# Performance work log

Hardware: AMD Instinct MI355X
Metric: run time of the kernel (lower is better)

The kernel has to match this reference:

```python
import jax, jax.numpy as jnp
import numpy as np

B, S, DIN, DQ, DK, NGL = 4, 8192, 512, 512, 512, 64


def setup_inputs() -> dict:
    key = jax.random.key(0)
    ks = jax.random.split(key, 10)
    q = jax.random.normal(ks[0], (B, S, DIN), dtype=jnp.float32)
    k = jax.random.normal(ks[1], (B, S, DIN), dtype=jnp.float32)
    v = jax.random.normal(ks[2], (B, S, DIN), dtype=jnp.float32)
    sc_in = 1.0 / np.sqrt(DIN)
    Wq = jax.random.normal(ks[3], (DQ, DIN), dtype=jnp.float32) * sc_in
    bq = jax.random.normal(ks[4], (DQ,), dtype=jnp.float32) * 0.01
    Wk = jax.random.normal(ks[5], (DK, DIN), dtype=jnp.float32) * sc_in
    bk = jax.random.normal(ks[6], (DK,), dtype=jnp.float32) * 0.01
    Wv = jax.random.normal(ks[7], (DK, DIN), dtype=jnp.float32) * sc_in
    bv = jax.random.normal(ks[8], (DK,), dtype=jnp.float32) * 0.01
    # deterministic stand-in for random.sample(range(DK), NGL): unique indices
    rng = np.random.default_rng(0)
    global_tokens = jnp.asarray(rng.choice(DK, size=NGL, replace=False), dtype=jnp.int32)
    return {"q": q, "k": k, "v": v, "Wq": Wq, "bq": bq, "Wk": Wk, "bk": bk,
            "Wv": Wv, "bv": bv, "global_tokens": global_tokens}


def _make_mask(global_tokens):
    # mask[a, b] = -inf iff a < b and neither a nor b is a global token
    idx = jnp.arange(DK)
    glb = jnp.zeros((DK,), dtype=bool).at[global_tokens].set(True)
    cond = (idx[:, None] < idx[None, :]) & (~glb[:, None]) & (~glb[None, :])
    return jnp.where(cond, -jnp.inf, 0.0).astype(jnp.float32)  # [DQ, DK]


def reference(q, k, v, Wq, bq, Wk, bk, Wv, bv, global_tokens):
    Q = q @ Wq.T + bq            # [B, S, DQ]
    K = k @ Wk.T + bk            # [B, S, DK]
    V = v @ Wv.T + bv            # [B, S, DK]
    # num = Q^T K contracting over the sequence axis -> [B, DQ, DK]
    num = jnp.einsum('bsq,bsk->bqk', Q, K)
    mask = _make_mask(global_tokens)
    denom = jnp.asarray(DK, jnp.float32) ** 0.5
    attn = jax.nn.softmax((num + mask) / denom, axis=-1)  # [B, DQ, DK]
    # attn @ V^T -> [B, DQ, S]
    out = jnp.einsum('bqk,bsk->bqs', attn, V)
    return out
```

## Files before the change

kernel.cpp:

```cpp
#include <hip/hip_runtime.h>
#include <stdint.h>

typedef short short8 __attribute__((ext_vector_type(8)));
typedef short short4v __attribute__((ext_vector_type(4)));
typedef float f32x4 __attribute__((ext_vector_type(4)));
typedef unsigned short ushort_t;

__device__ __forceinline__ unsigned short bf16_rne(float x){
  unsigned int u = __float_as_uint(x);
  return (unsigned short)((u + 0x7FFFu + ((u >> 16) & 1u)) >> 16);
}
__device__ __forceinline__ unsigned cvt_pk(float a, float b){
  unsigned r;
  asm("v_cvt_pk_bf16_f32 %0, %1, %2" : "=v"(r) : "v"(a), "v"(b));
  return r;
}
__device__ __forceinline__ void split4(float a0, float a1, float a2, float a3,
                                       unsigned &h0, unsigned &h1,
                                       unsigned &l0, unsigned &l1){
  h0 = cvt_pk(a0, a1); h1 = cvt_pk(a2, a3);
  float f0 = __uint_as_float(h0 << 16), f1 = __uint_as_float(h0 & 0xFFFF0000u);
  float f2 = __uint_as_float(h1 << 16), f3 = __uint_as_float(h1 & 0xFFFF0000u);
  l0 = cvt_pk(a0 - f0, a1 - f1); l1 = cvt_pk(a2 - f2, a3 - f3);
}
__device__ __forceinline__ uint4 hi8(float4 x, float4 y){
  uint4 h; h.x = cvt_pk(x.x, x.y); h.y = cvt_pk(x.z, x.w);
  h.z = cvt_pk(y.x, y.y); h.w = cvt_pk(y.z, y.w); return h;
}
__device__ __forceinline__ void split8(float4 x, float4 y, uint4 &h, uint4 &l){
  split4(x.x, x.y, x.z, x.w, h.x, h.y, l.x, l.y);
  split4(y.x, y.y, y.z, y.w, h.z, h.w, l.z, l.w);
}
__device__ __forceinline__ short8 comb(short4v a, short4v b){
  short8 r; r[0]=a[0]; r[1]=a[1]; r[2]=a[2]; r[3]=a[3];
  r[4]=b[0]; r[5]=b[1]; r[6]=b[2]; r[7]=b[3]; return r;
}

template<int TS, int ABF, int BBF, int NT, int EPI, int OB>
__global__ __launch_bounds__(256, 2) void gemm_bt(
    const void* __restrict__ Av, const void* __restrict__ Bv,
    void* __restrict__ Cv, const float* __restrict__ cvec,
    int tn, int K, int lda, int ldb, int ldc,
    long sA, long sB, long sC, long scv)
{
  const int bz = blockIdx.y;
  const int mt = blockIdx.x / tn, nt = blockIdx.x % tn;
  const int m0 = mt * TS, n0 = nt * TS;

  constexpr int MI   = TS / 64;
  constexpr int ROWE = TS * 32;
  constexpr int AL   = (NT == 3) ? 2 * ROWE : ROWE;
  constexpr int EL   = (TS == 128) ? 16 : 8;
  constexpr int SB   = (4 * AL > 16384) ? 4 * AL : 16384;
  __shared__ __align__(16) char SMEM[SB];
  short* Ah  = (short*)SMEM;
  short* Bh2 = (short*)(SMEM + 2 * AL);
  float* EP  = (float*)SMEM;

  const int t = threadIdx.x;
  const int lane = t & 63, wid = t >> 6;
  const int rowS = (TS == 128) ? (t >> 1) : (t >> 2);
  const int kh   = (TS == 128) ? (t & 1)  : (t & 3);
  const int wr = wid >> 1, wc = wid & 1;
  const int fr = lane & 15, fg = lane >> 4;

  f32x4 acc[2*MI][2*MI];
  const f32x4 Z = {0.f, 0.f, 0.f, 0.f};
  #pragma unroll
  for (int i = 0; i < 2*MI; i++)
    #pragma unroll
    for (int j = 0; j < 2*MI; j++) acc[i][j] = Z;

  const int wbase = rowS * 32;
  const int sw = (rowS >> 1) & 3;
  const int i0 = wbase + ((((TS == 128) ? (kh << 1) : kh) ^ sw) << 3);
  const int i1 = (TS == 128) ? (wbase + ((((kh << 1) + 1) ^ sw) << 3)) : 0;

  const float*    Afp = (const float*)Av    + sA * bz + (long)(m0 + rowS) * lda + kh * EL;
  const ushort_t* Abp = (const ushort_t*)Av + sA * bz + (long)(m0 + rowS) * lda + kh * EL;
  const float*    Bfp = (const float*)Bv    + sB * bz + (long)(n0 + rowS) * ldb + kh * EL;
  const ushort_t* Bbp = (const ushort_t*)Bv + sB * bz + (long)(n0 + rowS) * ldb + kh * EL;

  float4 a0, a1, a2, a3, b0, b1, b2, b3;
  short8 as0, as1, bs0, bs1;

  auto loadAB = [&](int kk){
    if (ABF == 0){
      const float4* pa = (const float4*)(Afp + kk);
      a0 = pa[0]; a1 = pa[1];
      if (TS == 128){ a2 = pa[2]; a3 = pa[3]; }
    } else {
      const short8* pa = (const short8*)(Abp + kk);
      as0 = pa[0]; if (TS == 128) as1 = pa[1];
    }
    if (BBF == 0){
      const float4* pb = (const float4*)(Bfp + kk);
      b0 = pb[0]; b1 = pb[1];
      if (TS == 128){ b2 = pb[2]; b3 = pb[3]; }
    } else {
      const short8* pb = (const short8*)(Bbp + kk);
      bs0 = pb[0]; if (TS == 128) bs1 = pb[1];
    }
  };

  loadAB(0);

  for (int k0 = 0; k0 < K; k0 += 32){
    __syncthreads();
    if (ABF == 0){
      if (NT == 3){
        uint4 h0, l0; split8(a0, a1, h0, l0);
        *(uint4*)&Ah[i0] = h0; *(uint4*)&Ah[i0 + ROWE] = l0;
        if (TS == 128){
          uint4 h1, l1; split8(a2, a3, h1, l1);
          *(uint4*)&Ah[i1] = h1; *(uint4*)&Ah[i1 + ROWE] = l1;
        }
      } else {
        *(uint4*)&Ah[i0] = hi8(a0, a1);
        if (TS == 128) *(uint4*)&Ah[i1] = hi8(a2, a3);
      }
    } else {
      *(short8*)&Ah[i0] = as0;
      if (TS == 128) *(short8*)&Ah[i1] = as1;
    }
    if (BBF == 0){
      if (NT == 3){
        uint4 h0, l0; split8(b0, b1, h0, l0);
        *(uint4*)&Bh2[i0] = h0; *(uint4*)&Bh2[i0 + ROWE] = l0;
        if (TS == 128){
          uint4 h1, l1; split8(b2, b3, h1, l1);
          *(uint4*)&Bh2[i1] = h1; *(uint4*)&Bh2[i1 + ROWE] = l1;
        }
      } else {
        *(uint4*)&Bh2[i0] = hi8(b0, b1);
        if (TS == 128) *(uint4*)&Bh2[i1] = hi8(b2, b3);
      }
    } else {
      *(short8*)&Bh2[i0] = bs0;
      if (TS == 128) *(short8*)&Bh2[i1] = bs1;
    }
    __syncthreads();

    loadAB((k0 + 32 < K) ? (k0 + 32) : k0);

    short8 fa[2*MI], fb[2*MI], fal[2*MI], fbl[2*MI];
    #pragma unroll
    for (int mi = 0; mi < 2*MI; mi++){
      int r = wr * (32*MI) + mi * 16 + fr;
      int idx = r * 32 + ((fg ^ ((r >> 1) & 3)) << 3);
      fa[mi] = *(const short8*)&Ah[idx];
      if (NT == 3) fal[mi] = *(const short8*)&Ah[idx + ROWE];
    }
    #pragma unroll
    for (int ni = 0; ni < 2*MI; ni++){
      int r = wc * (32*MI) + ni * 16 + fr;
      int idx = r * 32 + ((fg ^ ((r >> 1) & 3)) << 3);
      fb[ni] = *(const short8*)&Bh2[idx];
      if (NT == 3) fbl[ni] = *(const short8*)&Bh2[idx + ROWE];
    }
    #pragma unroll
    for (int mi = 0; mi < 2*MI; mi++)
      #pragma unroll
      for (int ni = 0; ni < 2*MI; ni++){
        acc[mi][ni] = __builtin_amdgcn_mfma_f32_16x16x32_bf16(fa[mi], fb[ni], acc[mi][ni], 0, 0, 0);
        if (NT == 3){
          acc[mi][ni] = __builtin_amdgcn_mfma_f32_16x16x32_bf16(fal[mi], fb[ni],  acc[mi][ni], 0, 0, 0);
          acc[mi][ni] = __builtin_amdgcn_mfma_f32_16x16x32_bf16(fa[mi],  fbl[ni], acc[mi][ni], 0, 0, 0);
        }
      }
  }

  float*    Cf = (float*)Cv    + sC * bz;
  ushort_t* Cb = (ushort_t*)Cv + sC * bz;
  if (TS == 128){
    #pragma unroll
    for (int p = 0; p < 4; p++){
      __syncthreads();
      if (wr == (p >> 1)){
        #pragma unroll
        for (int m2 = 0; m2 < 2; m2++){
          int mi = 2 * (p & 1) + m2;
          #pragma unroll
          for (int ni = 0; ni < 4; ni++)
            #pragma unroll
            for (int j = 0; j < 4; j++){
              int lr = m2 * 16 + fg * 4 + j;
              float o = acc[mi][ni][j];
              if (EPI == 1) o += cvec[scv * bz + m0 + p * 32 + lr];
              EP[lr * 128 + wc * 64 + ni * 16 + fr] = o;
            }
        }
      }
      __syncthreads();
      const int row = t >> 3, seg = t & 7;
      const float* src = EP + row * 128 + seg * 16;
      if (OB == 1){
        ushort_t* dst = Cb + (long)(m0 + p * 32 + row) * ldc + n0 + seg * 16;
        uint4 o0, o1;
        o0.x = cvt_pk(src[0], src[1]);  o0.y = cvt_pk(src[2], src[3]);
        o0.z = cvt_pk(src[4], src[5]);  o0.w = cvt_pk(src[6], src[7]);
        o1.x = cvt_pk(src[8], src[9]);  o1.y = cvt_pk(src[10], src[11]);
        o1.z = cvt_pk(src[12], src[13]); o1.w = cvt_pk(src[14], src[15]);
        *(uint4*)dst = o0; *(uint4*)(dst + 8) = o1;
      } else {
        float* dst = Cf + (long)(m0 + p * 32 + row) * ldc + n0 + seg * 16;
        #pragma unroll
        for (int c = 0; c < 4; c++)
          *(float4*)(dst + c * 4) = *(const float4*)(src + c * 4);
      }
    }
  } else {
    __syncthreads();
    #pragma unroll
    for (int mi = 0; mi < 2; mi++)
      #pragma unroll
      for (int ni = 0; ni < 2; ni++)
        #pragma unroll
        for (int j = 0; j < 4; j++){
          int lr = wr * 32 + mi * 16 + fg * 4 + j;
          float o = acc[mi][ni][j];
          if (EPI == 1) o += cvec[scv * bz + m0 + lr];
          EP[lr * 64 + wc * 32 + ni * 16 + fr] = o;
        }
    __syncthreads();
    const int row = t >> 2, seg = t & 3;
    const float* src = EP + row * 64 + seg * 16;
    if (OB == 1){
      ushort_t* dst = Cb + (long)(m0 + row) * ldc + n0 + seg * 16;
      uint4 o0, o1;
      o0.x = cvt_pk(src[0], src[1]);  o0.y = cvt_pk(src[2], src[3]);
      o0.z = cvt_pk(src[4], src[5]);  o0.w = cvt_pk(src[6], src[7]);
      o1.x = cvt_pk(src[8], src[9]);  o1.y = cvt_pk(src[10], src[11]);
      o1.z = cvt_pk(src[12], src[13]); o1.w = cvt_pk(src[14], src[15]);
      *(uint4*)dst = o0; *(uint4*)(dst + 8) = o1;
    } else {
      float* dst = Cf + (long)(m0 + row) * ldc + n0 + seg * 16;
      #pragma unroll
      for (int c = 0; c < 4; c++)
        *(float4*)(dst + c * 4) = *(const float4*)(src + c * 4);
    }
  }
}

template<int NSP>
__global__ __launch_bounds__(256, 2) void gemm1_tn(
    const float* __restrict__ q, const float* __restrict__ k,
    float* __restrict__ mtp, float* __restrict__ sqp, float* __restrict__ skp)
{
  constexpr int STEPS = 256 / NSP;
  const int b = blockIdx.z, sp = blockIdx.y;
  const int mt = blockIdx.x >> 2, nt = blockIdx.x & 3;
  const float* qb = q + (long)b * 8192 * 512;
  const float* kb = k + (long)b * 8192 * 512;

  __shared__ __align__(16) char SMEM[32768];
  unsigned char* As = (unsigned char*)SMEM;
  unsigned char* Bs = (unsigned char*)(SMEM + 16384);
  float* EP = (float*)SMEM;

  const int t = threadIdx.x;
  const int lam = t & 31, sg = t >> 5;
  const int lane = t & 63, wid = t >> 6;
  const int wr = wid >> 1, wc = wid & 1;
  const int fr = lane & 15, fg = lane >> 4;

  f32x4 acc[4][4];
  const f32x4 Z = {0.f, 0.f, 0.f, 0.f};
  #pragma unroll
  for (int i = 0; i < 4; i++)
    #pragma unroll
    for (int j = 0; j < 4; j++) acc[i][j] = Z;

  float sumk4[4] = {0.f, 0.f, 0.f, 0.f};
  float sumq4[4] = {0.f, 0.f, 0.f, 0.f};

  int wA[4];
  #pragma unroll
  for (int j = 0; j < 4; j++){
    int c = lam * 4 + j;
    int swc = ((c >> 2) ^ ((c & 3) << 1)) & 7;
    wA[j] = c * 128 + ((sg ^ swc) << 4);
  }

  const float* kbase = kb + (long)(sp * (STEPS * 32) + sg * 4) * 512 + mt * 128 + lam * 4;
  const float* qbase = qb + (long)(sp * (STEPS * 32) + sg * 4) * 512 + nt * 128 + lam * 4;

  float4 ka0 = *(const float4*)(kbase);
  float4 ka1 = *(const float4*)(kbase + 512);
  float4 ka2 = *(const float4*)(kbase + 1024);
  float4 ka3 = *(const float4*)(kbase + 1536);
  float4 qa0 = *(const float4*)(qbase);
  float4 qa1 = *(const float4*)(qbase + 512);
  float4 qa2 = *(const float4*)(qbase + 1024);
  float4 qa3 = *(const float4*)(qbase + 1536);

  for (int step = 0; step < STEPS; ++step){
    __syncthreads();
    #pragma unroll
    for (int j = 0; j < 4; j++){
      float a0 = ((const float*)&ka0)[j], a1 = ((const float*)&ka1)[j];
      float a2 = ((const float*)&ka2)[j], a3 = ((const float*)&ka3)[j];
      sumk4[j] += (a0 + a1) + (a2 + a3);
      unsigned h0, h1, l0, l1;
      split4(a0, a1, a2, a3, h0, h1, l0, l1);
      uint4 w; w.x = h0; w.y = h1; w.z = l0; w.w = l1;
      *(uint4*)(As + wA[j]) = w;
    }
    #pragma unroll
    for (int j = 0; j < 4; j++){
      float a0 = ((const float*)&qa0)[j], a1 = ((const float*)&qa1)[j];
      float a2 = ((const float*)&qa2)[j], a3 = ((const float*)&qa3)[j];
      sumq4[j] += (a0 + a1) + (a2 + a3);
      unsigned h0, h1, l0, l1;
      split4(a0, a1, a2, a3, h0, h1, l0, l1);
      uint4 w; w.x = h0; w.y = h1; w.z = l0; w.w = l1;
      *(uint4*)(Bs + wA[j]) = w;
    }
    __syncthreads();

    {
      const int nstep = (step < STEPS - 1) ? (step + 1) : step;
      const float* pK = kbase + (long)nstep * 16384;
      const float* pQ = qbase + (long)nstep * 16384;
      ka0 = *(const float4*)(pK);
      ka1 = *(const float4*)(pK + 512);
      ka2 = *(const float4*)(pK + 1024);
      ka3 = *(const float4*)(pK + 1536);
      qa0 = *(const float4*)(pQ);
      qa1 = *(const float4*)(pQ + 512);
      qa2 = *(const float4*)(pQ + 1024);
      qa3 = *(const float4*)(pQ + 1536);
    }

    short8 fa[4], fal[4], fb[4], fbl[4];
    #pragma unroll
    for (int mi = 0; mi < 4; mi++){
      int r = wr * 64 + mi * 16 + fr;
      int swc = ((r >> 2) ^ ((r & 3) << 1)) & 7;
      const unsigned char* bp = As + r * 128;
      int u0 = (((fg << 1) + 0) ^ swc) << 4;
      int u1 = (((fg << 1) + 1) ^ swc) << 4;
      fa[mi]  = comb(*(const short4v*)(bp + u0),     *(const short4v*)(bp + u1));
      fal[mi] = comb(*(const short4v*)(bp + u0 + 8), *(const short4v*)(bp + u1 + 8));
    }
    #pragma unroll
    for (int ni = 0; ni < 4; ni++){
      int r = wc * 64 + ni * 16 + fr;
      int swc = ((r >> 2) ^ ((r & 3) << 1)) & 7;
      const unsigned char* bp = Bs + r * 128;
      int u0 = (((fg << 1) + 0) ^ swc) << 4;
      int u1 = (((fg << 1) + 1) ^ swc) << 4;
      fb[ni]  = comb(*(const short4v*)(bp + u0),     *(const short4v*)(bp + u1));
      fbl[ni] = comb(*(const short4v*)(bp + u0 + 8), *(const short4v*)(bp + u1 + 8));
    }
    #pragma unroll
    for (int mi = 0; mi < 4; mi++)
      #pragma unroll
      for (int ni = 0; ni < 4; ni++){
        acc[mi][ni] = __builtin_amdgcn_mfma_f32_16x16x32_bf16(fa[mi],  fb[ni],  acc[mi][ni], 0, 0, 0);
        acc[mi][ni] = __builtin_amdgcn_mfma_f32_16x16x32_bf16(fal[mi], fb[ni],  acc[mi][ni], 0, 0, 0);
        acc[mi][ni] = __builtin_amdgcn_mfma_f32_16x16x32_bf16(fa[mi],  fbl[ni], acc[mi][ni], 0, 0, 0);
      }
  }

  float* Cp = mtp + ((long)sp * 4 + b) * (512 * 512);
  #pragma unroll
  for (int p = 0; p < 4; p++){
    __syncthreads();
    if (wr == (p >> 1)){
      #pragma unroll
      for (int m2 = 0; m2 < 2; m2++){
        int mi = 2 * (p & 1) + m2;
        #pragma unroll
        for (int ni = 0; ni < 4; ni++)
          #pragma unroll
          for (int j = 0; j < 4; j++){
            int lr = m2 * 16 + fg * 4 + j;
            EP[lr * 128 + wc * 64 + ni * 16 + fr] = acc[mi][ni][j];
          }
      }
    }
    __syncthreads();
    const int row = t >> 3, seg = t & 7;
    const float* src = EP + row * 128 + seg * 16;
    float* dst = Cp + (long)(mt * 128 + p * 32 + row) * 512 + nt * 128 + seg * 16;
    #pragma unroll
    for (int c = 0; c < 4; c++)
      *(float4*)(dst + c * 4) = *(const float4*)(src + c * 4);
  }

  __syncthreads();
  float* red = (float*)SMEM;
  if (mt == 0){
    #pragma unroll
    for (int j = 0; j < 4; j++) red[sg * 128 + lam * 4 + j] = sumq4[j];
    __syncthreads();
    if (t < 128){
      float s2 = 0.f;
      #pragma unroll
      for (int gg = 0; gg < 8; gg++) s2 += red[gg * 128 + t];
      sqp[((long)b * NSP + sp) * 512 + nt * 128 + t] = s2;
    }
    __syncthreads();
  }
  if (nt == 0){
    #pragma unroll
    for (int j = 0; j < 4; j++) red[sg * 128 + lam * 4 + j] = sumk4[j];
    __syncthreads();
    if (t < 128){
      float s2 = 0.f;
      #pragma unroll
      for (int gg = 0; gg < 8; gg++) s2 += red[gg * 128 + t];
      skp[((long)b * NSP + sp) * 512 + mt * 128 + t] = s2;
    }
  }
}

template<int NS>
__global__ __launch_bounds__(256) void reduceM(float* __restrict__ p){
  const int bid = blockIdx.x;
  const int b = bid >> 8;
  const long i = (long)(bid & 255) * 1024 + threadIdx.x * 4;
  float4 s = {0.f, 0.f, 0.f, 0.f};
  #pragma unroll
  for (int j = 0; j < NS; j++){
    float4 v = *(const float4*)(p + ((long)j * 4 + b) * 262144 + i);
    s.x += v.x; s.y += v.y; s.z += v.z; s.w += v.w;
  }
  *(float4*)(p + (long)b * 262144 + i) = s;
}

__global__ __launch_bounds__(256) void transpose512(const float* __restrict__ in, float* __restrict__ outp){
  __shared__ float tile[32][33];
  const int bx = blockIdx.x & 15, by = blockIdx.x >> 4;
  const int tx = threadIdx.x & 31, ty = threadIdx.x >> 5;
  #pragma unroll
  for (int r = 0; r < 4; r++)
    tile[ty + 8*r][tx] = in[(long)(by*32 + ty + 8*r) * 512 + bx*32 + tx];
  __syncthreads();
  #pragma unroll
  for (int r = 0; r < 4; r++)
    outp[(long)(bx*32 + ty + 8*r) * 512 + by*32 + tx] = tile[tx][ty + 8*r];
}

__global__ __launch_bounds__(256) void smallprep(
    const float* __restrict__ sqp, const float* __restrict__ skp,
    const float* __restrict__ Wq, const float* __restrict__ Wk,
    float* __restrict__ wqsq, float* __restrict__ wksk, int nsp)
{
  const int bid = blockIdx.x;
  const int tau = bid >> 4;
  const int b = (bid >> 2) & 3, ab = bid & 3;
  const float* P = tau ? skp : sqp;
  const float* W = tau ? Wk : Wq;
  float* O = tau ? wksk : wqsq;
  __shared__ float sv[512];
  const int t = threadIdx.x;
  for (int i = t; i < 512; i += 256){
    float s = 0.f;
    for (int g = 0; g < nsp; g++) s += P[((long)b * nsp + g) * 512 + i];
    sv[i] = s;
  }
  __syncthreads();
  const int a = ab * 128 + (t >> 1), half = t & 1;
  const float* Wr = W + (long)a * 512 + half * 256;
  const float* sp2 = sv + half * 256;
  float d = 0.f;
  #pragma unroll 8
  for (int j = 0; j < 256; j++) d += Wr[j] * sp2[j];
  d += __shfl_xor(d, 1);
  if (!half) O[(long)b * 512 + a] = d;
}

__global__ __launch_bounds__(256) void softmax_k(
    const float* __restrict__ num, float* __restrict__ attn, float* __restrict__ cv,
    const float* __restrict__ wqsq, const float* __restrict__ wksk,
    const float* __restrict__ bq, const float* __restrict__ bk,
    const float* __restrict__ bv, const int* __restrict__ gt)
{
  const int a = blockIdx.x, b = blockIdx.y;
  const int t = threadIdx.x;
  const int lane = t & 63, wid = t >> 6;
  __shared__ unsigned char gf[512];
  __shared__ float red[4];
  gf[t] = 0; gf[t + 256] = 0;
  __syncthreads();
  if (t < 64) gf[gt[t]] = 1;
  __syncthreads();

  const float* row = num + ((long)b * 512 + a) * 512;
  const float bqa = bq[a], wqa = wqsq[b * 512 + a];
  const int ga = gf[a];
  const int c0 = t, c1 = t + 256;
  float l0 = (row[c0] + wqa * bk[c0] + bqa * wksk[b*512 + c0] + 8192.0f * bqa * bk[c0]) * 0.04419417382415922f;
  float l1 = (row[c1] + wqa * bk[c1] + bqa * wksk[b*512 + c1] + 8192.0f * bqa * bk[c1]) * 0.04419417382415922f;
  if (a < c0 && !ga && !gf[c0]) l0 = -1e30f;
  if (a < c1 && !ga && !gf[c1]) l1 = -1e30f;

  float m = fmaxf(l0, l1);
  #pragma unroll
  for (int o = 32; o; o >>= 1) m = fmaxf(m, __shfl_xor(m, o));
  if (lane == 0) red[wid] = m;
  __syncthreads();
  m = fmaxf(fmaxf(red[0], red[1]), fmaxf(red[2], red[3]));
  __syncthreads();

  float e0 = __expf(l0 - m), e1 = __expf(l1 - m);
  float s = e0 + e1;
  #pragma unroll
  for (int o = 32; o; o >>= 1) s += __shfl_xor(s, o);
  if (lane == 0) red[wid] = s;
  __syncthreads();
  s = red[0] + red[1] + red[2] + red[3];
  __syncthreads();
  const float inv = 1.0f / s;
  const float a0 = e0 * inv, a1 = e1 * inv;
  float* arow = attn + ((long)b * 512 + a) * 512;
  arow[c0] = a0; arow[c1] = a1;

  float cp = a0 * bv[c0] + a1 * bv[c1];
  #pragma unroll
  for (int o = 32; o; o >>= 1) cp += __shfl_xor(cp, o);
  if (lane == 0) red[wid] = cp;
  __syncthreads();
  if (t == 0) cv[(long)b * 512 + a] = red[0] + red[1] + red[2] + red[3];
}

extern "C" void kernel_launch(void* const* d_in, const int* in_sizes, int n_in,
                              void* d_out, int out_size, void* d_ws, size_t ws_size,
                              hipStream_t stream) {
  const float* q  = (const float*)d_in[0];
  const float* k  = (const float*)d_in[1];
  const float* v  = (const float*)d_in[2];
  const float* Wq = (const float*)d_in[3];
  const float* bq = (const float*)d_in[4];
  const float* Wk = (const float*)d_in[5];
  const float* bk = (const float*)d_in[6];
  const float* Wv = (const float*)d_in[7];
  const float* bv = (const float*)d_in[8];
  const int*   gt = (const int*)d_in[9];
  float* out = (float*)d_out;

  const int NSP = 8;

  float* w = (float*)d_ws;
  float* MT   = w;
  float* T1   = w + 1048576;
  float* NUM  = w + 2097152;
  float* ATT  = w + 3145728;
  float* A2H  = w + 4194304;
  float* WVT  = A2H + 524288;
  float* SM   = w + (long)NSP * 1048576;
  float* SQP  = SM;
  float* SKP  = SQP + 32768;
  float* WQS  = SKP + 32768;
  float* WKS  = WQS + 2048;
  float* CV   = WKS + 2048;
  ushort_t* a2h = (ushort_t*)A2H;

  gemm1_tn<8><<<dim3(16, 8, 4), 256, 0, stream>>>(q, k, w, SQP, SKP);
  reduceM<8><<<1024, 256, 0, stream>>>(w);
  transpose512<<<256, 256, 0, stream>>>(Wv, WVT);
  smallprep<<<32, 256, 0, stream>>>(SQP, SKP, Wq, Wk, WQS, WKS, NSP);
  gemm_bt<64,0,0,3,0,0><<<dim3(64, 4), 256, 0, stream>>>(Wq, MT, T1, nullptr,
      8, 512, 512, 512, 512, 0L, 262144L, 262144L, 0L);
  gemm_bt<64,0,0,3,0,0><<<dim3(64, 4), 256, 0, stream>>>(T1, Wk, NUM, nullptr,
      8, 512, 512, 512, 512, 262144L, 0L, 262144L, 0L);
  softmax_k<<<dim3(512, 4), 256, 0, stream>>>(NUM, ATT, CV, WQS, WKS, bq, bk, bv, gt);
  gemm_bt<64,0,0,1,0,1><<<dim3(64, 4), 256, 0, stream>>>(ATT, WVT, a2h, nullptr,
      8, 512, 512, 512, 512, 262144L, 0L, 262144L, 0L);
  gemm_bt<128,1,0,1,1,0><<<dim3(256, 4), 256, 0, stream>>>(a2h, v, out, CV,
      64, 512, 512, 512, 8192, 262144L, 4194304L, 4194304L, 512L);
}
```

Measured before the change: 210.2 us.

## Process two K-chunks per barrier pair with doubled register prefetch in GEMMs

Both the generic gemm_bt and the gemm1_tn kernels now keep two sets of prefetched global tiles in registers and stage two 32-wide K slices into shared memory per iteration. This halves the number of __syncthreads pairs and gives more MFMA work between barriers. gemm1_tn also drops the LDS-staged epilogue and writes accumulators directly to global memory with scattered scalar stores. In exchange, register pressure and shared-memory use double (64KB in gemm1_tn), which may reduce occupancy below the launch bound of 2 blocks, and the direct stores are less coalesced.

Result: faster. 198.7 us (-5.5%).

```diff
diff --git a/kernel.cpp b/kernel.cpp
--- a/kernel.cpp
+++ b/kernel.cpp
@@ -49,12 +49,13 @@
 
   constexpr int MI   = TS / 64;
   constexpr int ROWE = TS * 32;
-  constexpr int AL   = (NT == 3) ? 2 * ROWE : ROWE;
+  constexpr int PL   = (NT == 3) ? 2 * ROWE : ROWE;
+  constexpr int TBYT = 4 * PL;
+  constexpr int SB   = (2 * TBYT > 16384) ? 2 * TBYT : 16384;
   constexpr int EL   = (TS == 128) ? 16 : 8;
-  constexpr int SB   = (4 * AL > 16384) ? 4 * AL : 16384;
   __shared__ __align__(16) char SMEM[SB];
   short* Ah  = (short*)SMEM;
-  short* Bh2 = (short*)(SMEM + 2 * AL);
+  short* Bh2 = (short*)(SMEM + TBYT);
   float* EP  = (float*)SMEM;
 
   const int t = threadIdx.x;
@@ -81,93 +82,106 @@
   const float*    Bfp = (const float*)Bv    + sB * bz + (long)(n0 + rowS) * ldb + kh * EL;
   const ushort_t* Bbp = (const ushort_t*)Bv + sB * bz + (long)(n0 + rowS) * ldb + kh * EL;
 
-  float4 a0, a1, a2, a3, b0, b1, b2, b3;
-  short8 as0, as1, bs0, bs1;
-
-  auto loadAB = [&](int kk){
+  struct Pf { float4 v[4]; };
+  struct Ps { short8 v[2]; };
+  Pf Af[2], Bf[2]; Ps As8[2], Bs8[2];
+
+  auto loadA = [&](int s, int kk){
     if (ABF == 0){
-      const float4* pa = (const float4*)(Afp + kk);
-      a0 = pa[0]; a1 = pa[1];
-      if (TS == 128){ a2 = pa[2]; a3 = pa[3]; }
+      const float4* p = (const float4*)(Afp + kk);
+      Af[s].v[0] = p[0]; Af[s].v[1] = p[1];
+      if (TS == 128){ Af[s].v[2] = p[2]; Af[s].v[3] = p[3]; }
     } else {
-      const short8* pa = (const short8*)(Abp + kk);
-      as0 = pa[0]; if (TS == 128) as1 = pa[1];
-    }
+      const short8* p = (const short8*)(Abp + kk);
+      As8[s].v[0] = p[0]; if (TS == 128) As8[s].v[1] = p[1];
+    }
+  };
+  auto loadB = [&](int s, int kk){
     if (BBF == 0){
-      const float4* pb = (const float4*)(Bfp + kk);
-      b0 = pb[0]; b1 = pb[1];
-      if (TS == 128){ b2 = pb[2]; b3 = pb[3]; }
+      const float4* p = (const float4*)(Bfp + kk);
+      Bf[s].v[0] = p[0]; Bf[s].v[1] = p[1];
+      if (TS == 128){ Bf[s].v[2] = p[2]; Bf[s].v[3] = p[3]; }
     } else {
-      const short8* pb = (const short8*)(Bbp + kk);
-      bs0 = pb[0]; if (TS == 128) bs1 = pb[1];
-    }
-  };
-
-  loadAB(0);
-
-  for (int k0 = 0; k0 < K; k0 += 32){
-    __syncthreads();
+      const short8* p = (const short8*)(Bbp + kk);
+      Bs8[s].v[0] = p[0]; if (TS == 128) Bs8[s].v[1] = p[1];
+    }
+  };
+
+  auto stage = [&](int s){
+    const int off = s * PL;
     if (ABF == 0){
       if (NT == 3){
-        uint4 h0, l0; split8(a0, a1, h0, l0);
-        *(uint4*)&Ah[i0] = h0; *(uint4*)&Ah[i0 + ROWE] = l0;
+        uint4 h0, l0; split8(Af[s].v[0], Af[s].v[1], h0, l0);
+        *(uint4*)&Ah[off + i0] = h0; *(uint4*)&Ah[off + i0 + ROWE] = l0;
         if (TS == 128){
-          uint4 h1, l1; split8(a2, a3, h1, l1);
-          *(uint4*)&Ah[i1] = h1; *(uint4*)&Ah[i1 + ROWE] = l1;
+          uint4 h1, l1; split8(Af[s].v[2], Af[s].v[3], h1, l1);
+          *(uint4*)&Ah[off + i1] = h1; *(uint4*)&Ah[off + i1 + ROWE] = l1;
         }
       } else {
-        *(uint4*)&Ah[i0] = hi8(a0, a1);
-        if (TS == 128) *(uint4*)&Ah[i1] = hi8(a2, a3);
+        *(uint4*)&Ah[off + i0] = hi8(Af[s].v[0], Af[s].v[1]);
+        if (TS == 128) *(uint4*)&Ah[off + i1] = hi8(Af[s].v[2], Af[s].v[3]);
       }
     } else {
-      *(short8*)&Ah[i0] = as0;
-      if (TS == 128) *(short8*)&Ah[i1] = as1;
+      *(short8*)&Ah[off + i0] = As8[s].v[0];
+      if (TS == 128) *(short8*)&Ah[off + i1] = As8[s].v[1];
     }
     if (BBF == 0){
       if (NT == 3){
-        uint4 h0, l0; split8(b0, b1, h0, l0);
-        *(uint4*)&Bh2[i0] = h0; *(uint4*)&Bh2[i0 + ROWE] = l0;
+        uint4 h0, l0; split8(Bf[s].v[0], Bf[s].v[1], h0, l0);
+        *(uint4*)&Bh2[off + i0] = h0; *(uint4*)&Bh2[off + i0 + ROWE] = l0;
         if (TS == 128){
-          uint4 h1, l1; split8(b2, b3, h1, l1);
-          *(uint4*)&Bh2[i1] = h1; *(uint4*)&Bh2[i1 + ROWE] = l1;
+          uint4 h1, l1; split8(Bf[s].v[2], Bf[s].v[3], h1, l1);
+          *(uint4*)&Bh2[off + i1] = h1; *(uint4*)&Bh2[off + i1 + ROWE] = l1;
         }
       } else {
-        *(uint4*)&Bh2[i0] = hi8(b0, b1);
-        if (TS == 128) *(uint4*)&Bh2[i1] = hi8(b2, b3);
+        *(uint4*)&Bh2[off + i0] = hi8(Bf[s].v[0], Bf[s].v[1]);
+        if (TS == 128) *(uint4*)&Bh2[off + i1] = hi8(Bf[s].v[2], Bf[s].v[3]);
       }
     } else {
-      *(short8*)&Bh2[i0] = bs0;
-      if (TS == 128) *(short8*)&Bh2[i1] = bs1;
-    }
-    __syncthreads();
-
-    loadAB((k0 + 32 < K) ? (k0 + 32) : k0);
-
-    short8 fa[2*MI], fb[2*MI], fal[2*MI], fbl[2*MI];
-    #pragma unroll
-    for (int mi = 0; mi < 2*MI; mi++){
-      int r = wr * (32*MI) + mi * 16 + fr;
-      int idx = r * 32 + ((fg ^ ((r >> 1) & 3)) << 3);
-      fa[mi] = *(const short8*)&Ah[idx];
-      if (NT == 3) fal[mi] = *(const short8*)&Ah[idx + ROWE];
-    }
-    #pragma unroll
-    for (int ni = 0; ni < 2*MI; ni++){
-      int r = wc * (32*MI) + ni * 16 + fr;
-      int idx = r * 32 + ((fg ^ ((r >> 1) & 3)) << 3);
-      fb[ni] = *(const short8*)&Bh2[idx];
-      if (NT == 3) fbl[ni] = *(const short8*)&Bh2[idx + ROWE];
-    }
-    #pragma unroll
-    for (int mi = 0; mi < 2*MI; mi++)
+      *(short8*)&Bh2[off + i0] = Bs8[s].v[0];
+      if (TS == 128) *(short8*)&Bh2[off + i1] = Bs8[s].v[1];
+    }
+  };
+
+  loadA(0, 0); loadB(0, 0); loadA(1, 32); loadB(1, 32);
+
+  for (int k0 = 0; k0 < K; k0 += 64){
+    __syncthreads();
+    stage(0);
+    { int kn = (k0 + 64 < K) ? (k0 + 64) : k0;       loadA(0, kn); loadB(0, kn); }
+    stage(1);
+    { int kn = (k0 + 64 < K) ? (k0 + 96) : (k0 + 32); loadA(1, kn); loadB(1, kn); }
+    __syncthreads();
+
+    #pragma unroll
+    for (int s = 0; s < 2; s++){
+      const int off = s * PL;
+      short8 fa[2*MI], fb[2*MI], fal[2*MI], fbl[2*MI];
+      #pragma unroll
+      for (int mi = 0; mi < 2*MI; mi++){
+        int r = wr * (32*MI) + mi * 16 + fr;
+        int idx = off + r * 32 + ((fg ^ ((r >> 1) & 3)) << 3);
+        fa[mi] = *(const short8*)&Ah[idx];
+        if (NT == 3) fal[mi] = *(const short8*)&Ah[idx + ROWE];
+      }
       #pragma unroll
       for (int ni = 0; ni < 2*MI; ni++){
-        acc[mi][ni] = __builtin_amdgcn_mfma_f32_16x16x32_bf16(fa[mi], fb[ni], acc[mi][ni], 0, 0, 0);
-        if (NT == 3){
-          acc[mi][ni] = __builtin_amdgcn_mfma_f32_16x16x32_bf16(fal[mi], fb[ni],  acc[mi][ni], 0, 0, 0);
-          acc[mi][ni] = __builtin_amdgcn_mfma_f32_16x16x32_bf16(fa[mi],  fbl[ni], acc[mi][ni], 0, 0, 0);
+        int r = wc * (32*MI) + ni * 16 + fr;
+        int idx = off + r * 32 + ((fg ^ ((r >> 1) & 3)) << 3);
+        fb[ni] = *(const short8*)&Bh2[idx];
+        if (NT == 3) fbl[ni] = *(const short8*)&Bh2[idx + ROWE];
+      }
+      #pragma unroll
+      for (int mi = 0; mi < 2*MI; mi++)
+        #pragma unroll
+        for (int ni = 0; ni < 2*MI; ni++){
+          acc[mi][ni] = __builtin_amdgcn_mfma_f32_16x16x32_bf16(fa[mi], fb[ni], acc[mi][ni], 0, 0, 0);
+          if (NT == 3){
+            acc[mi][ni] = __builtin_amdgcn_mfma_f32_16x16x32_bf16(fal[mi], fb[ni],  acc[mi][ni], 0, 0, 0);
+            acc[mi][ni] = __builtin_amdgcn_mfma_f32_16x16x32_bf16(fa[mi],  fbl[ni], acc[mi][ni], 0, 0, 0);
+          }
         }
-      }
+    }
   }
 
   float*    Cf = (float*)Cv    + sC * bz;
@@ -247,16 +261,16 @@
     const float* __restrict__ q, const float* __restrict__ k,
     float* __restrict__ mtp, float* __restrict__ sqp, float* __restrict__ skp)
 {
-  constexpr int STEPS = 256 / NSP;
+  constexpr int CH = 8192 / NSP;
+  constexpr int STEPS = CH / 64;
   const int b = blockIdx.z, sp = blockIdx.y;
   const int mt = blockIdx.x >> 2, nt = blockIdx.x & 3;
   const float* qb = q + (long)b * 8192 * 512;
   const float* kb = k + (long)b * 8192 * 512;
 
-  __shared__ __align__(16) char SMEM[32768];
+  __shared__ __align__(16) char SMEM[65536];
   unsigned char* As = (unsigned char*)SMEM;
-  unsigned char* Bs = (unsigned char*)(SMEM + 16384);
-  float* EP = (float*)SMEM;
+  unsigned char* Bs = (unsigned char*)(SMEM + 32768);
 
   const int t = threadIdx.x;
   const int lam = t & 31, sg = t >> 5;
@@ -282,112 +296,109 @@
     wA[j] = c * 128 + ((sg ^ swc) << 4);
   }
 
-  const float* kbase = kb + (long)(sp * (STEPS * 32) + sg * 4) * 512 + mt * 128 + lam * 4;
-  const float* qbase = qb + (long)(sp * (STEPS * 32) + sg * 4) * 512 + nt * 128 + lam * 4;
-
-  float4 ka0 = *(const float4*)(kbase);
-  float4 ka1 = *(const float4*)(kbase + 512);
-  float4 ka2 = *(const float4*)(kbase + 1024);
-  float4 ka3 = *(const float4*)(kbase + 1536);
-  float4 qa0 = *(const float4*)(qbase);
-  float4 qa1 = *(const float4*)(qbase + 512);
-  float4 qa2 = *(const float4*)(qbase + 1024);
-  float4 qa3 = *(const float4*)(qbase + 1536);
-
-  for (int step = 0; step < STEPS; ++step){
-    __syncthreads();
+  const float* kbase = kb + (long)(sp * CH + sg * 4) * 512 + mt * 128 + lam * 4;
+  const float* qbase = qb + (long)(sp * CH + sg * 4) * 512 + nt * 128 + lam * 4;
+
+  struct Pf { float4 v[4]; };
+  Pf Kf[2], Qf[2];
+
+  auto ldK = [&](int s, int st){
+    const float* p = kbase + (long)(st * 64 + s * 32) * 512;
+    Kf[s].v[0] = *(const float4*)(p);
+    Kf[s].v[1] = *(const float4*)(p + 512);
+    Kf[s].v[2] = *(const float4*)(p + 1024);
+    Kf[s].v[3] = *(const float4*)(p + 1536);
+  };
+  auto ldQ = [&](int s, int st){
+    const float* p = qbase + (long)(st * 64 + s * 32) * 512;
+    Qf[s].v[0] = *(const float4*)(p);
+    Qf[s].v[1] = *(const float4*)(p + 512);
+    Qf[s].v[2] = *(const float4*)(p + 1024);
+    Qf[s].v[3] = *(const float4*)(p + 1536);
+  };
+
+  auto cvK = [&](int s){
     #pragma unroll
     for (int j = 0; j < 4; j++){
-      float a0 = ((const float*)&ka0)[j], a1 = ((const float*)&ka1)[j];
-      float a2 = ((const float*)&ka2)[j], a3 = ((const float*)&ka3)[j];
+      float a0 = ((const float*)&Kf[s].v[0])[j], a1 = ((const float*)&Kf[s].v[1])[j];
+      float a2 = ((const float*)&Kf[s].v[2])[j], a3 = ((const float*)&Kf[s].v[3])[j];
       sumk4[j] += (a0 + a1) + (a2 + a3);
       unsigned h0, h1, l0, l1;
       split4(a0, a1, a2, a3, h0, h1, l0, l1);
       uint4 w; w.x = h0; w.y = h1; w.z = l0; w.w = l1;
-      *(uint4*)(As + wA[j]) = w;
-    }
+      *(uint4*)(As + s * 16384 + wA[j]) = w;
+    }
+  };
+  auto cvQ = [&](int s){
     #pragma unroll
     for (int j = 0; j < 4; j++){
-      float a0 = ((const float*)&qa0)[j], a1 = ((const float*)&qa1)[j];
-      float a2 = ((const float*)&qa2)[j], a3 = ((const float*)&qa3)[j];
+      float a0 = ((const float*)&Qf[s].v[0])[j], a1 = ((const float*)&Qf[s].v[1])[j];
+      float a2 = ((const float*)&Qf[s].v[2])[j], a3 = ((const float*)&Qf[s].v[3])[j];
       sumq4[j] += (a0 + a1) + (a2 + a3);
       unsigned h0, h1, l0, l1;
       split4(a0, a1, a2, a3, h0, h1, l0, l1);
       uint4 w; w.x = h0; w.y = h1; w.z = l0; w.w = l1;
-      *(uint4*)(Bs + wA[j]) = w;
-    }
-    __syncthreads();
-
-    {
-      const int nstep = (step < STEPS - 1) ? (step + 1) : step;
-      const float* pK = kbase + (long)nstep * 16384;
-      const float* pQ = qbase + (long)nstep * 16384;
-      ka0 = *(const float4*)(pK);
-      ka1 = *(const float4*)(pK + 512);
-      ka2 = *(const float4*)(pK + 1024);
-      ka3 = *(const float4*)(pK + 1536);
-      qa0 = *(const float4*)(pQ);
-      qa1 = *(const float4*)(pQ + 512);
-      qa2 = *(const float4*)(pQ + 1024);
-      qa3 = *(const float4*)(pQ + 1536);
-    }
-
-    short8 fa[4], fal[4], fb[4], fbl[4];
-    #pragma unroll
-    for (int mi = 0; mi < 4; mi++){
-      int r = wr * 64 + mi * 16 + fr;
-      int swc = ((r >> 2) ^ ((r & 3) << 1)) & 7;
-      const unsigned char* bp = As + r * 128;
-      int u0 = (((fg << 1) + 0) ^ swc) << 4;
-      int u1 = (((fg << 1) + 1) ^ swc) << 4;
-      fa[mi]  = comb(*(const short4v*)(bp + u0),     *(const short4v*)(bp + u1));
-      fal[mi] = comb(*(const short4v*)(bp + u0 + 8), *(const short4v*)(bp + u1 + 8));
-    }
+      *(uint4*)(Bs + s * 16384 + wA[j]) = w;
+    }
+  };
+
+  ldK(0, 0); ldQ(0, 0); ldK(1, 0); ldQ(1, 0);
+
+  for (int st = 0; st < STEPS; ++st){
+    __syncthreads();
+    cvK(0); cvQ(0);
+    { int ns = (st < STEPS - 1) ? (st + 1) : st; ldK(0, ns); ldQ(0, ns); }
+    cvK(1); cvQ(1);
+    { int ns = (st < STEPS - 1) ? (st + 1) : st; ldK(1, ns); ldQ(1, ns); }
+    __syncthreads();
+
+    #pragma unroll
+    for (int s = 0; s < 2; s++){
+      const unsigned char* Ab = As + s * 16384;
+      const unsigned char* Bb = Bs + s * 16384;
+      short8 fa[4], fal[4], fb[4], fbl[4];
+      #pragma unroll
+      for (int mi = 0; mi < 4; mi++){
+        int r = wr * 64 + mi * 16 + fr;
+        int swc = ((r >> 2) ^ ((r & 3) << 1)) & 7;
+        const unsigned char* bp = Ab + r * 128;
+        int u0 = (((fg << 1) + 0) ^ swc) << 4;
+        int u1 = (((fg << 1) + 1) ^ swc) << 4;
+        fa[mi]  = comb(*(const short4v*)(bp + u0),     *(const short4v*)(bp + u1));
+        fal[mi] = comb(*(const short4v*)(bp + u0 + 8), *(const short4v*)(bp + u1 + 8));
+      }
+      #pragma unroll
+      for (int ni = 0; ni < 4; ni++){
+        int r = wc * 64 + ni * 16 + fr;
+        int swc = ((r >> 2) ^ ((r & 3) << 1)) & 7;
+        const unsigned char* bp = Bb + r * 128;
+        int u0 = (((fg << 1) + 0) ^ swc) << 4;
+        int u1 = (((fg << 1) + 1) ^ swc) << 4;
+        fb[ni]  = comb(*(const short4v*)(bp + u0),     *(const short4v*)(bp + u1));
+        fbl[ni] = comb(*(const short4v*)(bp + u0 + 8), *(const short4v*)(bp + u1 + 8));
+      }
+      #pragma unroll
+      for (int mi = 0; mi < 4; mi++)
+        #pragma unroll
+        for (int ni = 0; ni < 4; ni++){
+          acc[mi][ni] = __builtin_amdgcn_mfma_f32_16x16x32_bf16(fa[mi],  fb[ni],  acc[mi][ni], 0, 0, 0);
+          acc[mi][ni] = __builtin_amdgcn_mfma_f32_16x16x32_bf16(fal[mi], fb[ni],  acc[mi][ni], 0, 0, 0);
+          acc[mi][ni] = __builtin_amdgcn_mfma_f32_16x16x32_bf16(fa[mi],  fbl[ni], acc[mi][ni], 0, 0, 0);
+        }
+    }
+  }
+
+  float* Cp = mtp + ((long)sp * 4 + b) * (512 * 512);
+  #pragma unroll
+  for (int mi = 0; mi < 4; mi++)
     #pragma unroll
     for (int ni = 0; ni < 4; ni++){
-      int r = wc * 64 + ni * 16 + fr;
-      int swc = ((r >> 2) ^ ((r & 3) << 1)) & 7;
-      const unsigned char* bp = Bs + r * 128;
-      int u0 = (((fg << 1) + 0) ^ swc) << 4;
-      int u1 = (((fg << 1) + 1) ^ swc) << 4;
-      fb[ni]  = comb(*(const short4v*)(bp + u0),     *(const short4v*)(bp + u1));
-      fbl[ni] = comb(*(const short4v*)(bp + u0 + 8), *(const short4v*)(bp + u1 + 8));
-    }
-    #pragma unroll
-    for (int mi = 0; mi < 4; mi++)
-      #pragma unroll
-      for (int ni = 0; ni < 4; ni++){
-        acc[mi][ni] = __builtin_amdgcn_mfma_f32_16x16x32_bf16(fa[mi],  fb[ni],  acc[mi][ni], 0, 0, 0);
-        acc[mi][ni] = __builtin_amdgcn_mfma_f32_16x16x32_bf16(fal[mi], fb[ni],  acc[mi][ni], 0, 0, 0);
-        acc[mi][ni] = __builtin_amdgcn_mfma_f32_16x16x32_bf16(fa[mi],  fbl[ni], acc[mi][ni], 0, 0, 0);
-      }
-  }
-
-  float* Cp = mtp + ((long)sp * 4 + b) * (512 * 512);
-  #pragma unroll
-  for (int p = 0; p < 4; p++){
-    __syncthreads();
-    if (wr == (p >> 1)){
-      #pragma unroll
-      for (int m2 = 0; m2 < 2; m2++){
-        int mi = 2 * (p & 1) + m2;
-        #pragma unroll
-        for (int ni = 0; ni < 4; ni++)
-          #pragma unroll
-          for (int j = 0; j < 4; j++){
-            int lr = m2 * 16 + fg * 4 + j;
-            EP[lr * 128 + wc * 64 + ni * 16 + fr] = acc[mi][ni][j];
-          }
-      }
-    }
-    __syncthreads();
-    const int row = t >> 3, seg = t & 7;
-    const float* src = EP + row * 128 + seg * 16;
-    float* dst = Cp + (long)(mt * 128 + p * 32 + row) * 512 + nt * 128 + seg * 16;
-    #pragma unroll
-    for (int c = 0; c < 4; c++)
-      *(float4*)(dst + c * 4) = *(const float4*)(src + c * 4);
-  }
+      int gr0 = mt * 128 + wr * 64 + mi * 16 + fg * 4;
+      int gc  = nt * 128 + wc * 64 + ni * 16 + fr;
+      #pragma unroll
+      for (int j = 0; j < 4; j++)
+        Cp[(long)(gr0 + j) * 512 + gc] = acc[mi][ni][j];
+    }
 
   __syncthreads();
   float* red = (float*)SMEM;
```
